# Kernel optimization log

Hardware: AMD Instinct MI355X
Metric: run time of the kernel (lower is better)

## Reference

```python
import jax, jax.numpy as jnp
import numpy as np

N = 8192
F_IN = 128
F_OUT = 64
NEG_INF = -9e15


def setup_inputs() -> dict:
    key = jax.random.key(0)
    k1, k2, k3, k4 = jax.random.split(key, 4)
    x = jax.random.normal(k1, (N, F_IN), dtype=jnp.float32)
    adj = jax.random.randint(k2, (N, N), 0, 2, dtype=jnp.int32)
    W = jax.random.normal(k3, (F_OUT, F_IN), dtype=jnp.float32) * 0.05  # torch Linear weight [out,in]
    a = jax.random.normal(k4, (1, 2 * F_OUT), dtype=jnp.float32) * 0.05  # attention vector weight [1, 2*out]
    return {"x": x, "adj": adj, "W": W, "a": a}


def reference(x, adj, W, a):
    fout = W.shape[0]
    Wh = x @ W.T                                   # [N, out]
    a1 = a[0, :fout]                               # a.weight.T[:out]
    a2 = a[0, fout:]                               # a.weight.T[out:]
    Wh1 = Wh @ a1                                  # [N]
    Wh2 = Wh @ a2                                  # [N]
    e = jax.nn.leaky_relu(Wh1[:, None] + Wh2[None, :], negative_slope=0.2)  # [N, N]
    attention = jnp.where(adj > 0, e, NEG_INF)
    attention = jax.nn.softmax(attention, axis=1)
    # dropout is identity in eval / deterministic reference
    h_prime = attention @ Wh                       # [N, out]
    return jax.nn.elu(h_prime)
```

## Files before the change

kernel.cpp:

```cpp
#include <hip/hip_runtime.h>
#include <hip/hip_bf16.h>
#include <cstdint>
#include <cstddef>

#define NN 8192
#define FIN 128
#define FOUT 64

typedef __attribute__((ext_vector_type(8))) short short8;
typedef __attribute__((ext_vector_type(4))) float f32x4;

__device__ __forceinline__ unsigned short f32_to_bf16_bits(float f) {
    union { float f; uint32_t u; } c; c.f = f;
    uint32_t u = c.u;
    u += 0x7fffu + ((u >> 16) & 1u);
    return (unsigned short)(u >> 16);
}

__global__ __launch_bounds__(256) void gat_prep(
    const float* __restrict__ x, const float* __restrict__ W,
    const float* __restrict__ a, unsigned short* __restrict__ WhT,
    float* __restrict__ Wh1, float* __restrict__ Wh2)
{
    const int t    = threadIdx.x;
    const int f    = t & 63;
    const int iloc = t >> 6;
    const int i    = blockIdx.x * 4 + iloc;

    const float4* x4 = (const float4*)(x + (size_t)i * FIN);
    const float4* w4 = (const float4*)(W + (size_t)f * FIN);

    float acc = 0.f;
#pragma unroll
    for (int k = 0; k < FIN / 4; ++k) {
        float4 xv = x4[k];
        float4 wv = w4[k];
        acc += xv.x * wv.x + xv.y * wv.y + xv.z * wv.z + xv.w * wv.w;
    }

    WhT[(size_t)f * NN + i] = f32_to_bf16_bits(acc);

    float r1 = acc * a[f];
    float r2 = acc * a[64 + f];
#pragma unroll
    for (int m = 1; m < 64; m <<= 1) {
        r1 += __shfl_xor(r1, m, 64);
        r2 += __shfl_xor(r2, m, 64);
    }
    if (f == 0) { Wh1[i] = r1; Wh2[i] = r2; }
}

__global__ __launch_bounds__(512, 4) void gat_attn(
    const int* __restrict__ adj, const unsigned short* __restrict__ WhT,
    const float* __restrict__ Wh1, const float* __restrict__ Wh2,
    float* __restrict__ out)
{
    __shared__ float lds_C[8][16][68];
    __shared__ float lds_tot[8][16];

    const int tid  = threadIdx.x;
    const int wave = tid >> 6;
    const int lane = tid & 63;
    const int il   = lane & 15;
    const int q    = lane >> 4;
    const int i0   = blockIdx.x * 16;
    const int i    = i0 + il;

    const float wh1   = Wh1[i];
    const int   jbase = wave * 32 + q * 8;
    const int* __restrict__ adjrow = adj + (size_t)i * NN;

    const short8* bp0 = (const short8*)(WhT + (size_t)(0  + il) * NN);
    const short8* bp1 = (const short8*)(WhT + (size_t)(16 + il) * NN);
    const short8* bp2 = (const short8*)(WhT + (size_t)(32 + il) * NN);
    const short8* bp3 = (const short8*)(WhT + (size_t)(48 + il) * NN);

    f32x4 acc0 = {0.f, 0.f, 0.f, 0.f};
    f32x4 acc1 = {0.f, 0.f, 0.f, 0.f};
    f32x4 acc2 = {0.f, 0.f, 0.f, 0.f};
    f32x4 acc3 = {0.f, 0.f, 0.f, 0.f};
    float tot0 = 0.f, tot1 = 0.f;

    int4   aA0 = *(const int4*)(adjrow + jbase);
    int4   aA1 = *(const int4*)(adjrow + jbase + 4);
    int4   aB0 = *(const int4*)(adjrow + jbase + 256);
    int4   aB1 = *(const int4*)(adjrow + jbase + 260);
    int4   aC0 = *(const int4*)(adjrow + jbase + 512);
    int4   aC1 = *(const int4*)(adjrow + jbase + 516);
    float4 wA0 = *(const float4*)(Wh2 + jbase);
    float4 wA1 = *(const float4*)(Wh2 + jbase + 4);

#pragma unroll 1
    for (int tt = 0; tt < 32; ++tt) {
        const int jn3 = jbase + (((tt + 3) & 31) << 8);
        const int4 nav0 = *(const int4*)(adjrow + jn3);
        const int4 nav1 = *(const int4*)(adjrow + jn3 + 4);

        const int jn1 = jbase + (((tt + 1) & 31) << 8);
        const float4 nw20 = *(const float4*)(Wh2 + jn1);
        const float4 nw21 = *(const float4*)(Wh2 + jn1 + 4);

        const int jb = (jbase + (tt << 8)) >> 3;
        const short8 b0 = bp0[jb];
        const short8 b1 = bp1[jb];
        const short8 b2 = bp2[jb];
        const short8 b3 = bp3[jb];

        float wv[8];
#define CALC(idx, adjv, wh2v, totv)                                    \
        {                                                              \
            float s = wh1 + (wh2v);                                    \
            float e = fmaxf(s, 0.2f * s);          \
            float v = ((adjv) > 0) ? __expf(e) : 0.f;                  \
            totv += v;                                                 \
            wv[idx] = v;                                               \
        }
        CALC(0, aA0.x, wA0.x, tot0) CALC(1, aA0.y, wA0.y, tot1)
        CALC(2, aA0.z, wA0.z, tot0) CALC(3, aA0.w, wA0.w, tot1)
        CALC(4, aA1.x, wA1.x, tot0) CALC(5, aA1.y, wA1.y, tot1)
        CALC(6, aA1.z, wA1.z, tot0) CALC(7, aA1.w, wA1.w, tot1)
#undef CALC

        union { short8 v; __hip_bfloat162 h[4]; } af;
        af.h[0] = __float22bfloat162_rn(float2{wv[0], wv[1]});
        af.h[1] = __float22bfloat162_rn(float2{wv[2], wv[3]});
        af.h[2] = __float22bfloat162_rn(float2{wv[4], wv[5]});
        af.h[3] = __float22bfloat162_rn(float2{wv[6], wv[7]});

        acc0 = __builtin_amdgcn_mfma_f32_16x16x32_bf16(af.v, b0, acc0, 0, 0, 0);
        acc1 = __builtin_amdgcn_mfma_f32_16x16x32_bf16(af.v, b1, acc1, 0, 0, 0);
        acc2 = __builtin_amdgcn_mfma_f32_16x16x32_bf16(af.v, b2, acc2, 0, 0, 0);
        acc3 = __builtin_amdgcn_mfma_f32_16x16x32_bf16(af.v, b3, acc3, 0, 0, 0);

        aA0 = aB0; aA1 = aB1;
        aB0 = aC0; aB1 = aC1;
        aC0 = nav0; aC1 = nav1;
        wA0 = nw20; wA1 = nw21;
    }

    float tot = tot0 + tot1;
    tot += __shfl_xor(tot, 16, 64);
    tot += __shfl_xor(tot, 32, 64);
    if (lane < 16) lds_tot[wave][lane] = tot;

#pragma unroll
    for (int r = 0; r < 4; ++r) {
        lds_C[wave][q * 4 + r][0 * 16 + il] = acc0[r];
        lds_C[wave][q * 4 + r][1 * 16 + il] = acc1[r];
        lds_C[wave][q * 4 + r][2 * 16 + il] = acc2[r];
        lds_C[wave][q * 4 + r][3 * 16 + il] = acc3[r];
    }
    __syncthreads();

#pragma unroll
    for (int e = 0; e < 2; ++e) {
        const int idx = e * 512 + tid;
        const int ii = idx >> 6;
        const int ff = idx & 63;
        float s = 0.f;
#pragma unroll
        for (int w = 0; w < 8; ++w) s += lds_C[w][ii][ff];
        float t = lds_tot[0][ii] + lds_tot[1][ii] + lds_tot[2][ii] +
                  lds_tot[3][ii] + lds_tot[4][ii] + lds_tot[5][ii] +
                  lds_tot[6][ii] + lds_tot[7][ii];
        const float p = s / t;
        out[(size_t)(i0 + ii) * FOUT + ff] = (p > 0.f) ? p : (__expf(p) - 1.f);
    }
}

extern "C" void kernel_launch(void* const* d_in, const int* in_sizes, int n_in,
                              void* d_out, int out_size, void* d_ws, size_t ws_size,
                              hipStream_t stream) {
    const float* x   = (const float*)d_in[0];
    const int*   adj = (const int*)d_in[1];
    const float* W   = (const float*)d_in[2];
    const float* a   = (const float*)d_in[3];
    float* out = (float*)d_out;

    char* ws = (char*)d_ws;
    unsigned short* WhT = (unsigned short*)ws;
    float* Wh1   = (float*)(ws + (size_t)1048576);
    float* Wh2   = (float*)(ws + (size_t)1048576 + 32768);

    gat_prep<<<dim3(NN / 4), dim3(256), 0, stream>>>(x, W, a, WhT, Wh1, Wh2);
    gat_attn<<<dim3(NN / 16), dim3(512), 0, stream>>>(adj, WhT, Wh1, Wh2, out);
}
```

Before: 435.1 us.

## Process two 16-row groups per wave to share WhT and Wh2 loads

The attention kernel now handles 32 rows per block with 1024 threads, so each wave computes two 16-row MFMA tiles that reuse the same WhT B-fragments and Wh2 values. This halves the per-row global loads of WhT and Wh2. The j-loop takes 512-column strides over 16 iterations. Adjacency prefetch depth drops from three stages to one, while LDS for the reduction grows substantially. Larger blocks and more accumulator registers may lower occupancy and expose adj load latency.

```diff
diff --git a/kernel.cpp b/kernel.cpp
--- a/kernel.cpp
+++ b/kernel.cpp
@@ -50,25 +50,28 @@
     if (f == 0) { Wh1[i] = r1; Wh2[i] = r2; }
 }
 
-__global__ __launch_bounds__(512, 4) void gat_attn(
+__global__ __launch_bounds__(1024, 4) void gat_attn(
     const int* __restrict__ adj, const unsigned short* __restrict__ WhT,
     const float* __restrict__ Wh1, const float* __restrict__ Wh2,
     float* __restrict__ out)
 {
-    __shared__ float lds_C[8][16][68];
-    __shared__ float lds_tot[8][16];
+    __shared__ float lds_C[16][32][66];
+    __shared__ float lds_tot[16][32];
 
     const int tid  = threadIdx.x;
     const int wave = tid >> 6;
     const int lane = tid & 63;
     const int il   = lane & 15;
     const int q    = lane >> 4;
-    const int i0   = blockIdx.x * 16;
-    const int i    = i0 + il;
-
-    const float wh1   = Wh1[i];
+    const int i0   = blockIdx.x * 32;
+    const int iA   = i0 + il;
+    const int iB   = i0 + 16 + il;
+
+    const float wh1A = Wh1[iA];
+    const float wh1B = Wh1[iB];
     const int   jbase = wave * 32 + q * 8;
-    const int* __restrict__ adjrow = adj + (size_t)i * NN;
+    const int* __restrict__ adjA = adj + (size_t)iA * NN;
+    const int* __restrict__ adjB = adj + (size_t)iB * NN;
 
     const short8* bp0 = (const short8*)(WhT + (size_t)(0  + il) * NN);
     const short8* bp1 = (const short8*)(WhT + (size_t)(16 + il) * NN);
@@ -79,69 +82,84 @@
     f32x4 acc1 = {0.f, 0.f, 0.f, 0.f};
     f32x4 acc2 = {0.f, 0.f, 0.f, 0.f};
     f32x4 acc3 = {0.f, 0.f, 0.f, 0.f};
-    float tot0 = 0.f, tot1 = 0.f;
-
-    int4   aA0 = *(const int4*)(adjrow + jbase);
-    int4   aA1 = *(const int4*)(adjrow + jbase + 4);
-    int4   aB0 = *(const int4*)(adjrow + jbase + 256);
-    int4   aB1 = *(const int4*)(adjrow + jbase + 260);
-    int4   aC0 = *(const int4*)(adjrow + jbase + 512);
-    int4   aC1 = *(const int4*)(adjrow + jbase + 516);
-    float4 wA0 = *(const float4*)(Wh2 + jbase);
-    float4 wA1 = *(const float4*)(Wh2 + jbase + 4);
+    f32x4 acc4 = {0.f, 0.f, 0.f, 0.f};
+    f32x4 acc5 = {0.f, 0.f, 0.f, 0.f};
+    f32x4 acc6 = {0.f, 0.f, 0.f, 0.f};
+    f32x4 acc7 = {0.f, 0.f, 0.f, 0.f};
+    float totA = 0.f, totB = 0.f;
+
+    int4 avA0 = *(const int4*)(adjA + jbase);
+    int4 avA1 = *(const int4*)(adjA + jbase + 4);
+    int4 avB0 = *(const int4*)(adjB + jbase);
+    int4 avB1 = *(const int4*)(adjB + jbase + 4);
 
 #pragma unroll 1
-    for (int tt = 0; tt < 32; ++tt) {
-        const int jn3 = jbase + (((tt + 3) & 31) << 8);
-        const int4 nav0 = *(const int4*)(adjrow + jn3);
-        const int4 nav1 = *(const int4*)(adjrow + jn3 + 4);
-
-        const int jn1 = jbase + (((tt + 1) & 31) << 8);
-        const float4 nw20 = *(const float4*)(Wh2 + jn1);
-        const float4 nw21 = *(const float4*)(Wh2 + jn1 + 4);
-
-        const int jb = (jbase + (tt << 8)) >> 3;
+    for (int tt = 0; tt < 16; ++tt) {
+        const int jn = jbase + (((tt + 1) & 15) << 9);
+        const int4 nA0 = *(const int4*)(adjA + jn);
+        const int4 nA1 = *(const int4*)(adjA + jn + 4);
+        const int4 nB0 = *(const int4*)(adjB + jn);
+        const int4 nB1 = *(const int4*)(adjB + jn + 4);
+
+        const int j  = jbase + (tt << 9);
+        const float4 w20 = *(const float4*)(Wh2 + j);
+        const float4 w21 = *(const float4*)(Wh2 + j + 4);
+        const int jb = j >> 3;
         const short8 b0 = bp0[jb];
         const short8 b1 = bp1[jb];
         const short8 b2 = bp2[jb];
         const short8 b3 = bp3[jb];
 
         float wv[8];
-#define CALC(idx, adjv, wh2v, totv)                                    \
+#define CALC(idx, adjv, wh1v, wh2v, totv)                              \
         {                                                              \
-            float s = wh1 + (wh2v);                                    \
+            float s = (wh1v) + (wh2v);                                 \
             float e = fmaxf(s, 0.2f * s);          \
             float v = ((adjv) > 0) ? __expf(e) : 0.f;                  \
             totv += v;                                                 \
             wv[idx] = v;                                               \
         }
-        CALC(0, aA0.x, wA0.x, tot0) CALC(1, aA0.y, wA0.y, tot1)
-        CALC(2, aA0.z, wA0.z, tot0) CALC(3, aA0.w, wA0.w, tot1)
-        CALC(4, aA1.x, wA1.x, tot0) CALC(5, aA1.y, wA1.y, tot1)
-        CALC(6, aA1.z, wA1.z, tot0) CALC(7, aA1.w, wA1.w, tot1)
+        CALC(0, avA0.x, wh1A, w20.x, totA) CALC(1, avA0.y, wh1A, w20.y, totA)
+        CALC(2, avA0.z, wh1A, w20.z, totA) CALC(3, avA0.w, wh1A, w20.w, totA)
+        CALC(4, avA1.x, wh1A, w21.x, totA) CALC(5, avA1.y, wh1A, w21.y, totA)
+        CALC(6, avA1.z, wh1A, w21.z, totA) CALC(7, avA1.w, wh1A, w21.w, totA)
+        union { short8 v; __hip_bfloat162 h[4]; } afA;
+        afA.h[0] = __float22bfloat162_rn(float2{wv[0], wv[1]});
+        afA.h[1] = __float22bfloat162_rn(float2{wv[2], wv[3]});
+        afA.h[2] = __float22bfloat162_rn(float2{wv[4], wv[5]});
+        afA.h[3] = __float22bfloat162_rn(float2{wv[6], wv[7]});
+
+        CALC(0, avB0.x, wh1B, w20.x, totB) CALC(1, avB0.y, wh1B, w20.y, totB)
+        CALC(2, avB0.z, wh1B, w20.z, totB) CALC(3, avB0.w, wh1B, w20.w, totB)
+        CALC(4, avB1.x, wh1B, w21.x, totB) CALC(5, avB1.y, wh1B, w21.y, totB)
+        CALC(6, avB1.z, wh1B, w21.z, totB) CALC(7, avB1.w, wh1B, w21.w, totB)
 #undef CALC
-
-        union { short8 v; __hip_bfloat162 h[4]; } af;
-        af.h[0] = __float22bfloat162_rn(float2{wv[0], wv[1]});
-        af.h[1] = __float22bfloat162_rn(float2{wv[2], wv[3]});
-        af.h[2] = __float22bfloat162_rn(float2{wv[4], wv[5]});
-        af.h[3] = __float22bfloat162_rn(float2{wv[6], wv[7]});
-
-        acc0 = __builtin_amdgcn_mfma_f32_16x16x32_bf16(af.v, b0, acc0, 0, 0, 0);
-        acc1 = __builtin_amdgcn_mfma_f32_16x16x32_bf16(af.v, b1, acc1, 0, 0, 0);
-        acc2 = __builtin_amdgcn_mfma_f32_16x16x32_bf16(af.v, b2, acc2, 0, 0, 0);
-        acc3 = __builtin_amdgcn_mfma_f32_16x16x32_bf16(af.v, b3, acc3, 0, 0, 0);
-
-        aA0 = aB0; aA1 = aB1;
-        aB0 = aC0; aB1 = aC1;
-        aC0 = nav0; aC1 = nav1;
-        wA0 = nw20; wA1 = nw21;
-    }
-
-    float tot = tot0 + tot1;
-    tot += __shfl_xor(tot, 16, 64);
-    tot += __shfl_xor(tot, 32, 64);
-    if (lane < 16) lds_tot[wave][lane] = tot;
+        union { short8 v; __hip_bfloat162 h[4]; } afB;
+        afB.h[0] = __float22bfloat162_rn(float2{wv[0], wv[1]});
+        afB.h[1] = __float22bfloat162_rn(float2{wv[2], wv[3]});
+        afB.h[2] = __float22bfloat162_rn(float2{wv[4], wv[5]});
+        afB.h[3] = __float22bfloat162_rn(float2{wv[6], wv[7]});
+
+        acc0 = __builtin_amdgcn_mfma_f32_16x16x32_bf16(afA.v, b0, acc0, 0, 0, 0);
+        acc1 = __builtin_amdgcn_mfma_f32_16x16x32_bf16(afA.v, b1, acc1, 0, 0, 0);
+        acc2 = __builtin_amdgcn_mfma_f32_16x16x32_bf16(afA.v, b2, acc2, 0, 0, 0);
+        acc3 = __builtin_amdgcn_mfma_f32_16x16x32_bf16(afA.v, b3, acc3, 0, 0, 0);
+        acc4 = __builtin_amdgcn_mfma_f32_16x16x32_bf16(afB.v, b0, acc4, 0, 0, 0);
+        acc5 = __builtin_amdgcn_mfma_f32_16x16x32_bf16(afB.v, b1, acc5, 0, 0, 0);
+        acc6 = __builtin_amdgcn_mfma_f32_16x16x32_bf16(afB.v, b2, acc6, 0, 0, 0);
+        acc7 = __builtin_amdgcn_mfma_f32_16x16x32_bf16(afB.v, b3, acc7, 0, 0, 0);
+
+        avA0 = nA0; avA1 = nA1; avB0 = nB0; avB1 = nB1;
+    }
+
+    totA += __shfl_xor(totA, 16, 64);
+    totA += __shfl_xor(totA, 32, 64);
+    totB += __shfl_xor(totB, 16, 64);
+    totB += __shfl_xor(totB, 32, 64);
+    if (lane < 16) {
+        lds_tot[wave][lane]      = totA;
+        lds_tot[wave][16 + lane] = totB;
+    }
 
 #pragma unroll
     for (int r = 0; r < 4; ++r) {
@@ -149,20 +167,25 @@
         lds_C[wave][q * 4 + r][1 * 16 + il] = acc1[r];
         lds_C[wave][q * 4 + r][2 * 16 + il] = acc2[r];
         lds_C[wave][q * 4 + r][3 * 16 + il] = acc3[r];
+        lds_C[wave][16 + q * 4 + r][0 * 16 + il] = acc4[r];
+        lds_C[wave][16 + q * 4 + r][1 * 16 + il] = acc5[r];
+        lds_C[wave][16 + q * 4 + r][2 * 16 + il] = acc6[r];
+        lds_C[wave][16 + q * 4 + r][3 * 16 + il] = acc7[r];
     }
     __syncthreads();
 
 #pragma unroll
     for (int e = 0; e < 2; ++e) {
-        const int idx = e * 512 + tid;
+        const int idx = e * 1024 + tid;
         const int ii = idx >> 6;
         const int ff = idx & 63;
         float s = 0.f;
-#pragma unroll
-        for (int w = 0; w < 8; ++w) s += lds_C[w][ii][ff];
-        float t = lds_tot[0][ii] + lds_tot[1][ii] + lds_tot[2][ii] +
-                  lds_tot[3][ii] + lds_tot[4][ii] + lds_tot[5][ii] +
-                  lds_tot[6][ii] + lds_tot[7][ii];
+        float t = 0.f;
+#pragma unroll
+        for (int w = 0; w < 16; ++w) {
+            s += lds_C[w][ii][ff];
+            t += lds_tot[w][ii];
+        }
         const float p = s / t;
         out[(size_t)(i0 + ii) * FOUT + ff] = (p > 0.f) ? p : (__expf(p) - 1.f);
     }
@@ -183,5 +206,5 @@
     float* Wh2   = (float*)(ws + (size_t)1048576 + 32768);
 
     gat_prep<<<dim3(NN / 4), dim3(256), 0, stream>>>(x, W, a, WhT, Wh1, Wh2);
-    gat_attn<<<dim3(NN / 16), dim3(512), 0, stream>>>(adj, WhT, Wh1, Wh2, out);
-}
+    gat_attn<<<dim3(NN / 32), dim3(1024), 0, stream>>>(adj, WhT, Wh1, Wh2, out);
+}
```

Measured after the change: 425.2 us. -2.3%, faster.
